# Kernel tuning notes

Measured on AMD Instinct MI355X. Metric: run time of the kernel, lower is better.

## Reference

```python
import jax, jax.numpy as jnp
import numpy as np

H = 3.0        # args.h smoothing length
N_NODES = 100000
DIM_HIDDEN = 128
D = 3


def setup_inputs() -> dict:
    key = jax.random.key(0)
    ks = jax.random.split(key, 10)
    E = 1600000
    v = jax.random.normal(ks[0], (N_NODES, D), dtype=jnp.float32)
    r_ij = jax.random.normal(ks[1], (E, D), dtype=jnp.float32)
    edge_index = jax.random.randint(ks[2], (2, E), 0, N_NODES, dtype=jnp.int64)
    # teacher MLP params: [1+D] -> dim_hidden -> dim_hidden -> 1
    def lin(k, fan_in, fan_out):
        bound = 1.0 / np.sqrt(fan_in)
        kw, kb = jax.random.split(k)
        W = jax.random.uniform(kw, (fan_out, fan_in), jnp.float32, -bound, bound)
        b = jax.random.uniform(kb, (fan_out,), jnp.float32, -bound, bound)
        return W, b
    W0, b0 = lin(ks[3], 1 + D, DIM_HIDDEN)
    W1, b1 = lin(ks[4], DIM_HIDDEN, DIM_HIDDEN)
    W2, b2 = lin(ks[5], DIM_HIDDEN, 1)
    return {"v": v, "r_ij": r_ij, "W0": W0, "b0": b0, "W1": W1, "b1": b1,
            "W2": W2, "b2": b2, "edge_index": edge_index}


def _teacher(x, W0, b0, W1, b1, W2, b2):
    x = jax.nn.silu(x @ W0.T + b0)
    x = jax.nn.silu(x @ W1.T + b1)
    return x @ W2.T + b2  # [E, 1]


def _scatter_mean(x, idx, n):
    s = jax.ops.segment_sum(x, idx, num_segments=n)
    c = jax.ops.segment_sum(jnp.ones((idx.shape[0], 1), x.dtype), idx, num_segments=n)
    return s / jnp.maximum(c, 1.0)


def reference(v, r_ij, W0, b0, W1, b1, W2, b2, edge_index):
    i = edge_index[0]
    j = edge_index[1]
    v_ij = v[i] - v[j]                                   # [E, D] gather-diff
    r_ = jnp.sqrt(jnp.sum(r_ij * r_ij, axis=-1, keepdims=True)) / H  # [E, 1]
    m_i = _teacher(jnp.concatenate([r_, v_ij], axis=-1), W0, b0, W1, b1, W2, b2)
    m_j = _teacher(jnp.concatenate([r_, -v_ij], axis=-1), W0, b0, W1, b1, W2, b2)
    S = _scatter_mean(m_i, i, N_NODES) + _scatter_mean(m_j, j, N_NODES)  # [N, 1]
    return S
```

## Files before the change

### kernel.cpp

```cpp
#include <hip/hip_runtime.h>

typedef unsigned short ushort_t;
typedef __bf16 bf16x8 __attribute__((ext_vector_type(8)));
typedef __bf16 bf16x2 __attribute__((ext_vector_type(2)));
typedef float f32x4 __attribute__((ext_vector_type(4)));

#define LOG2E 1.4426950408889634f
#define LN2   0.6931471805599453f

__device__ __forceinline__ ushort_t f2bf(float f) {
    unsigned u;
    __builtin_memcpy(&u, &f, 4);
    u += 0x7fffu + ((u >> 16) & 1u);
    return (ushort_t)(u >> 16);
}

__device__ __forceinline__ float silu2(float y) {
    float e = __builtin_amdgcn_exp2f(-y);
    return y * __builtin_amdgcn_rcpf(1.0f + e);
}

__device__ __forceinline__ float rdlane(float v, int l) {
    return __builtin_bit_cast(float, __builtin_amdgcn_readlane(__builtin_bit_cast(int, v), l));
}


#define CNT_UNIT 65536.0

__global__ __launch_bounds__(256, 3) void mlp_kernel(
    const float* __restrict__ v,
    const float* __restrict__ rij,
    const float* __restrict__ W0,
    const float* __restrict__ b0,
    const float* __restrict__ W1,
    const float* __restrict__ b1,
    const float* __restrict__ W2,
    const float* __restrict__ b2,
    const int* __restrict__ eidx,
    double* __restrict__ acc_i, double* __restrict__ acc_j,
    int E, int nchunks)
{
    __shared__ ushort_t sW1[16384];
    __shared__ ushort_t sH0[8192];

    const int tid  = threadIdx.x;
    const int lane = tid & 63;
    const int wave = tid >> 6;

    {
        int n = tid >> 1, half = tid & 1;
        const float* src = W1 + n * 128;
#pragma unroll
        for (int dk = 0; dk < 8; dk++) {
            int k0   = half * 64 + dk * 8;
            int frag = (n >> 4) * 4 + (k0 >> 5);
            int slot = (n & 15) + 16 * ((k0 >> 3) & 3);
            ushort_t tmp[8];
#pragma unroll
            for (int t = 0; t < 8; t++) tmp[t] = f2bf(src[k0 + t]);
            *(uint4*)(&sW1[frag * 512 + slot * 8]) = *(const uint4*)tmp;
        }
    }

    float4 w0q[2]; float b0v[2];
#pragma unroll
    for (int kk = 0; kk < 2; kk++) {
        int h = 2 * lane + kk;
        w0q[kk].x = W0[h * 4 + 0] * LOG2E;
        w0q[kk].y = W0[h * 4 + 1] * LOG2E;
        w0q[kk].z = W0[h * 4 + 2] * LOG2E;
        w0q[kk].w = W0[h * 4 + 3] * LOG2E;
        b0v[kk]   = b0[h] * LOG2E;
    }
    float b1v[8], w2v[8];
#pragma unroll
    for (int nt = 0; nt < 8; nt++) {
        int ccol = nt * 16 + (lane & 15);
        b1v[nt] = b1[ccol] * LOG2E;
        w2v[nt] = W2[ccol] * LN2;
    }
    const float b2f = b2[0];

    __syncthreads();

    const int q = lane >> 4, c = lane & 15, p = (lane >> 2) & 3, bsub = lane & 3;
    const int ple  = lane >> 2;
    const int comp = lane & 3;

    auto preload = [&](int ch, float& val_o, int& idx_o) {
        float val = 0.f; int idxr = 0;
        int pe = ch * 64 + wave * 16 + ple;
        if (ch < nchunks && pe < E) {
            if (comp == 3) {
                float r0 = rij[3 * pe], r1 = rij[3 * pe + 1], r2 = rij[3 * pe + 2];
                val = sqrtf(fmaf(r0, r0, fmaf(r1, r1, r2 * r2))) * (1.0f / 3.0f);
            } else {
                int i = eidx[pe], jj = eidx[E + pe];
                idxr = (comp == 1) ? jj : i;
                val = v[3 * i + comp] - v[3 * jj + comp];
            }
        }
        val_o = val; idx_o = idxr;
    };

    float val; int idxr;
    preload(blockIdx.x, val, idxr);

    for (int chunk = blockIdx.x; chunk < nchunks; chunk += gridDim.x) {
        const float val_cur = val;
        const int   idx_cur = idxr;
        preload(chunk + (int)gridDim.x, val, idxr);

        const int ebase = chunk * 64 + wave * 16;

        bf16x8 afr[2][4];
#pragma unroll
        for (int half = 0; half < 2; ++half) {
#pragma unroll
            for (int le = 0; le < 8; le++) {
                int se = half * 8 + le;
                float vx = rdlane(val_cur, se * 4 + 0);
                float vy = rdlane(val_cur, se * 4 + 1);
                float vz = rdlane(val_cur, se * 4 + 2);
                float rr = rdlane(val_cur, se * 4 + 3);
                float si_[2], sj_[2];
#pragma unroll
                for (int kk = 0; kk < 2; kk++) {
                    float cc = fmaf(w0q[kk].x, rr, b0v[kk]);
                    float dd = fmaf(w0q[kk].y, vx, fmaf(w0q[kk].z, vy, w0q[kk].w * vz));
                    si_[kk] = silu2(cc + dd);
                    sj_[kk] = silu2(cc - dd);
                }
                bf16x2 pki, pkj;
                pki[0] = (__bf16)si_[0]; pki[1] = (__bf16)si_[1];
                pkj[0] = (__bf16)sj_[0]; pkj[1] = (__bf16)sj_[1];
                int mi = 2 * le;
                int fr = wave * 4 + q;
                int sli = ((mi ^ q ^ (p << 2)) & 15) + (p << 4);
                int slj = (((mi + 1) ^ q ^ (p << 2)) & 15) + (p << 4);
                ((unsigned*)sH0)[fr * 256 + sli * 4 + bsub] = __builtin_bit_cast(unsigned, pki);
                ((unsigned*)sH0)[fr * 256 + slj * 4 + bsub] = __builtin_bit_cast(unsigned, pkj);
            }
#pragma unroll
            for (int ks = 0; ks < 4; ks++) {
                int sl_rd = (((lane & 15) ^ ks ^ (q << 2)) & 15) + 16 * q;
                afr[half][ks] = *(const bf16x8*)(&sH0[(wave * 4 + ks) * 512 + sl_rd * 8]);
            }
        }

        f32x4 acc[2][8];
#pragma unroll
        for (int t = 0; t < 2; t++)
#pragma unroll
            for (int nt = 0; nt < 8; nt++)
                acc[t][nt] = (f32x4){b1v[nt], b1v[nt], b1v[nt], b1v[nt]};

#pragma unroll
        for (int ks = 0; ks < 4; ks++) {
#pragma unroll
            for (int nt = 0; nt < 8; nt++) {
                bf16x8 bb = *(const bf16x8*)(&sW1[(nt * 4 + ks) * 512 + lane * 8]);
                acc[0][nt] = __builtin_amdgcn_mfma_f32_16x16x32_bf16(afr[0][ks], bb, acc[0][nt], 0, 0, 0);
                acc[1][nt] = __builtin_amdgcn_mfma_f32_16x16x32_bf16(afr[1][ks], bb, acc[1][nt], 0, 0, 0);
            }
        }

        float rs[2][4] = {{0.f, 0.f, 0.f, 0.f}, {0.f, 0.f, 0.f, 0.f}};
#pragma unroll
        for (int t = 0; t < 2; t++)
#pragma unroll
            for (int nt = 0; nt < 8; nt++)
#pragma unroll
                for (int r = 0; r < 4; r++) {
                    float x = acc[t][nt][r];
                    rs[t][r] = fmaf(silu2(x), w2v[nt], rs[t][r]);
                }
#pragma unroll
        for (int t = 0; t < 2; t++)
#pragma unroll
            for (int r = 0; r < 4; r++) {
                float s = rs[t][r];
                s += __shfl_xor(s, 1, 64);
                s += __shfl_xor(s, 2, 64);
                s += __shfl_xor(s, 4, 64);
                s += __shfl_xor(s, 8, 64);
                int el  = t * 8 + q * 2 + (r >> 1);
                int src = el * 4 + (r & 1);
                int node = __shfl(idx_cur, src, 64);
                int e = ebase + el;
                if (c == 0 && e < E) {
                    double contrib = (double)(s + b2f) + CNT_UNIT;
                    if (r & 1) atomicAdd(&acc_j[node], contrib);
                    else       atomicAdd(&acc_i[node], contrib);
                }
            }
    }
}

__global__ void finalize_kernel(const double* __restrict__ acc_i,
                                const double* __restrict__ acc_j,
                                float* __restrict__ out, int N)
{
    int n = blockIdx.x * 256 + threadIdx.x;
    if (n < N) {
        double ti = acc_i[n], tj = acc_j[n];
        double ci = rint(ti * (1.0 / CNT_UNIT));
        double cj = rint(tj * (1.0 / CNT_UNIT));
        double si = ti - ci * CNT_UNIT;
        double sj = tj - cj * CNT_UNIT;
        out[n] = (float)(si / fmax(ci, 1.0) + sj / fmax(cj, 1.0));
    }
}

extern "C" void kernel_launch(void* const* d_in, const int* in_sizes, int n_in,
                              void* d_out, int out_size, void* d_ws, size_t ws_size,
                              hipStream_t stream) {
    const float* v   = (const float*)d_in[0];
    const float* rij = (const float*)d_in[1];
    const float* W0  = (const float*)d_in[2];
    const float* b0  = (const float*)d_in[3];
    const float* W1  = (const float*)d_in[4];
    const float* b1  = (const float*)d_in[5];
    const float* W2  = (const float*)d_in[6];
    const float* b2  = (const float*)d_in[7];
    const int* eidx  = (const int*)d_in[8];

    const int E = in_sizes[1] / 3;
    const int N = out_size;

    double* acc_i = (double*)d_ws;
    double* acc_j = acc_i + N;

    hipMemsetAsync(d_ws, 0, (size_t)2 * N * sizeof(double), stream);

    int nchunks = (E + 63) / 64;
    int grid = nchunks < 768 ? nchunks : 768;
    mlp_kernel<<<grid, 256, 0, stream>>>(v, rij, W0, b0, W1, b1, W2, b2, eidx,
                                         acc_i, acc_j, E, nchunks);
    finalize_kernel<<<(N + 255) / 256, 256, 0, stream>>>(acc_i, acc_j,
                                                         (float*)d_out, N);
}
```

Before: 381.1 us.

## Batch SiLU reciprocals four-at-a-time and enlarge blocks to 512 threads

Replaces the per-element SiLU reciprocal with a shared reciprocal across four values (one rcp plus extra multiplies), clamping inputs so the product of denominators cannot overflow. Also doubles the block to 512 threads (8 waves, 128 edges per chunk), sharing the bf16 W1 tile in LDS across more waves and changing the grid to 512 blocks with launch bounds (512,4). The aim is to cut transcendental-unit pressure and amortize W1 staging, at the cost of extra VALU multiplies, a slight precision change, and a different occupancy and register budget.

```diff
diff --git a/kernel.cpp b/kernel.cpp
--- a/kernel.cpp
+++ b/kernel.cpp
@@ -15,9 +15,20 @@
     return (ushort_t)(u >> 16);
 }
 
-__device__ __forceinline__ float silu2(float y) {
-    float e = __builtin_amdgcn_exp2f(-y);
-    return y * __builtin_amdgcn_rcpf(1.0f + e);
+__device__ __forceinline__ void silu2x4(float y0, float y1, float y2, float y3,
+                                        float& o0, float& o1, float& o2, float& o3) {
+    float e0 = __builtin_amdgcn_exp2f(-fmaxf(y0, -30.0f));
+    float e1 = __builtin_amdgcn_exp2f(-fmaxf(y1, -30.0f));
+    float e2 = __builtin_amdgcn_exp2f(-fmaxf(y2, -30.0f));
+    float e3 = __builtin_amdgcn_exp2f(-fmaxf(y3, -30.0f));
+    float d0 = 1.0f + e0, d1 = 1.0f + e1, d2 = 1.0f + e2, d3 = 1.0f + e3;
+    float p01 = d0 * d1, p23 = d2 * d3;
+    float r   = __builtin_amdgcn_rcpf(p01 * p23);
+    float r01 = p23 * r, r23 = p01 * r;
+    o0 = y0 * (d1 * r01);
+    o1 = y1 * (d0 * r01);
+    o2 = y2 * (d3 * r23);
+    o3 = y3 * (d2 * r23);
 }
 
 __device__ __forceinline__ float rdlane(float v, int l) {
@@ -27,7 +38,7 @@
 
 #define CNT_UNIT 65536.0
 
-__global__ __launch_bounds__(256, 3) void mlp_kernel(
+__global__ __launch_bounds__(512, 4) void mlp_kernel(
     const float* __restrict__ v,
     const float* __restrict__ rij,
     const float* __restrict__ W0,
@@ -41,18 +52,18 @@
     int E, int nchunks)
 {
     __shared__ ushort_t sW1[16384];
-    __shared__ ushort_t sH0[8192];
+    __shared__ ushort_t sH0[16384];
 
     const int tid  = threadIdx.x;
     const int lane = tid & 63;
     const int wave = tid >> 6;
 
     {
-        int n = tid >> 1, half = tid & 1;
+        int n = tid >> 2, qr = tid & 3;
         const float* src = W1 + n * 128;
 #pragma unroll
-        for (int dk = 0; dk < 8; dk++) {
-            int k0   = half * 64 + dk * 8;
+        for (int dk = 0; dk < 4; dk++) {
+            int k0   = qr * 32 + dk * 8;
             int frag = (n >> 4) * 4 + (k0 >> 5);
             int slot = (n & 15) + 16 * ((k0 >> 3) & 3);
             ushort_t tmp[8];
@@ -89,7 +100,7 @@
 
     auto preload = [&](int ch, float& val_o, int& idx_o) {
         float val = 0.f; int idxr = 0;
-        int pe = ch * 64 + wave * 16 + ple;
+        int pe = ch * 128 + wave * 16 + ple;
         if (ch < nchunks && pe < E) {
             if (comp == 3) {
                 float r0 = rij[3 * pe], r1 = rij[3 * pe + 1], r2 = rij[3 * pe + 2];
@@ -111,7 +122,7 @@
         const int   idx_cur = idxr;
         preload(chunk + (int)gridDim.x, val, idxr);
 
-        const int ebase = chunk * 64 + wave * 16;
+        const int ebase = chunk * 128 + wave * 16;
 
         bf16x8 afr[2][4];
 #pragma unroll
@@ -123,17 +134,15 @@
                 float vy = rdlane(val_cur, se * 4 + 1);
                 float vz = rdlane(val_cur, se * 4 + 2);
                 float rr = rdlane(val_cur, se * 4 + 3);
-                float si_[2], sj_[2];
-#pragma unroll
-                for (int kk = 0; kk < 2; kk++) {
-                    float cc = fmaf(w0q[kk].x, rr, b0v[kk]);
-                    float dd = fmaf(w0q[kk].y, vx, fmaf(w0q[kk].z, vy, w0q[kk].w * vz));
-                    si_[kk] = silu2(cc + dd);
-                    sj_[kk] = silu2(cc - dd);
-                }
+                float cc0 = fmaf(w0q[0].x, rr, b0v[0]);
+                float dd0 = fmaf(w0q[0].y, vx, fmaf(w0q[0].z, vy, w0q[0].w * vz));
+                float cc1 = fmaf(w0q[1].x, rr, b0v[1]);
+                float dd1 = fmaf(w0q[1].y, vx, fmaf(w0q[1].z, vy, w0q[1].w * vz));
+                float s0, s1, s2, s3;
+                silu2x4(cc0 + dd0, cc0 - dd0, cc1 + dd1, cc1 - dd1, s0, s1, s2, s3);
                 bf16x2 pki, pkj;
-                pki[0] = (__bf16)si_[0]; pki[1] = (__bf16)si_[1];
-                pkj[0] = (__bf16)sj_[0]; pkj[1] = (__bf16)sj_[1];
+                pki[0] = (__bf16)s0; pki[1] = (__bf16)s2;
+                pkj[0] = (__bf16)s1; pkj[1] = (__bf16)s3;
                 int mi = 2 * le;
                 int fr = wave * 4 + q;
                 int sli = ((mi ^ q ^ (p << 2)) & 15) + (p << 4);
@@ -169,12 +178,15 @@
 #pragma unroll
         for (int t = 0; t < 2; t++)
 #pragma unroll
-            for (int nt = 0; nt < 8; nt++)
-#pragma unroll
-                for (int r = 0; r < 4; r++) {
-                    float x = acc[t][nt][r];
-                    rs[t][r] = fmaf(silu2(x), w2v[nt], rs[t][r]);
-                }
+            for (int nt = 0; nt < 8; nt++) {
+                float s0, s1, s2, s3;
+                silu2x4(acc[t][nt][0], acc[t][nt][1], acc[t][nt][2], acc[t][nt][3],
+                        s0, s1, s2, s3);
+                rs[t][0] = fmaf(s0, w2v[nt], rs[t][0]);
+                rs[t][1] = fmaf(s1, w2v[nt], rs[t][1]);
+                rs[t][2] = fmaf(s2, w2v[nt], rs[t][2]);
+                rs[t][3] = fmaf(s3, w2v[nt], rs[t][3]);
+            }
 #pragma unroll
         for (int t = 0; t < 2; t++)
 #pragma unroll
@@ -233,9 +245,9 @@
 
     hipMemsetAsync(d_ws, 0, (size_t)2 * N * sizeof(double), stream);
 
-    int nchunks = (E + 63) / 64;
-    int grid = nchunks < 768 ? nchunks : 768;
-    mlp_kernel<<<grid, 256, 0, stream>>>(v, rij, W0, b0, W1, b1, W2, b2, eidx,
+    int nchunks = (E + 127) / 128;
+    int grid = nchunks < 512 ? nchunks : 512;
+    mlp_kernel<<<grid, 512, 0, stream>>>(v, rij, W0, b0, W1, b1, W2, b2, eidx,
                                          acc_i, acc_j, E, nchunks);
     finalize_kernel<<<(N + 255) / 256, 256, 0, stream>>>(acc_i, acc_j,
                                                          (float*)d_out, N);
```

After: 492.1 us. 29.1% more time.

## Swap MFMA operands so hidden units map to rows, shrinking output reduction

Applied to the files above, without the earlier changes.

Swaps the A/B operands of the second-layer MFMA so each accumulator holds hidden units along rows and edge-rows along columns. The layer-2 dot product then reduces mostly within each lane's registers, needing only two cross-lane shuffles per output instead of four per register-slot, and cuts 16 shuffle/atomic iterations to 2. Bias and W2 move from per-lane register arrays to shared memory, read as float4 per tile, which frees registers at the cost of extra LDS reads inside the hot loop.

```diff
diff --git a/kernel.cpp b/kernel.cpp
--- a/kernel.cpp
+++ b/kernel.cpp
@@ -42,6 +42,8 @@
 {
     __shared__ ushort_t sW1[16384];
     __shared__ ushort_t sH0[8192];
+    __shared__ float    sB1[128];
+    __shared__ float    sW2[128];
 
     const int tid  = threadIdx.x;
     const int lane = tid & 63;
@@ -60,6 +62,10 @@
             for (int t = 0; t < 8; t++) tmp[t] = f2bf(src[k0 + t]);
             *(uint4*)(&sW1[frag * 512 + slot * 8]) = *(const uint4*)tmp;
         }
+    }
+    if (tid < 128) {
+        sB1[tid] = b1[tid] * LOG2E;
+        sW2[tid] = W2[tid] * LN2;
     }
 
     float4 w0q[2]; float b0v[2];
@@ -72,18 +78,12 @@
         w0q[kk].w = W0[h * 4 + 3] * LOG2E;
         b0v[kk]   = b0[h] * LOG2E;
     }
-    float b1v[8], w2v[8];
-#pragma unroll
-    for (int nt = 0; nt < 8; nt++) {
-        int ccol = nt * 16 + (lane & 15);
-        b1v[nt] = b1[ccol] * LOG2E;
-        w2v[nt] = W2[ccol] * LN2;
-    }
     const float b2f = b2[0];
 
     __syncthreads();
 
     const int q = lane >> 4, c = lane & 15, p = (lane >> 2) & 3, bsub = lane & 3;
+    const int q4 = q * 4;
     const int ple  = lane >> 2;
     const int comp = lane & 3;
 
@@ -123,17 +123,17 @@
                 float vy = rdlane(val_cur, se * 4 + 1);
                 float vz = rdlane(val_cur, se * 4 + 2);
                 float rr = rdlane(val_cur, se * 4 + 3);
-                float si_[2], sj_[2];
-#pragma unroll
-                for (int kk = 0; kk < 2; kk++) {
-                    float cc = fmaf(w0q[kk].x, rr, b0v[kk]);
-                    float dd = fmaf(w0q[kk].y, vx, fmaf(w0q[kk].z, vy, w0q[kk].w * vz));
-                    si_[kk] = silu2(cc + dd);
-                    sj_[kk] = silu2(cc - dd);
-                }
+                float cc0 = fmaf(w0q[0].x, rr, b0v[0]);
+                float dd0 = fmaf(w0q[0].y, vx, fmaf(w0q[0].z, vy, w0q[0].w * vz));
+                float cc1 = fmaf(w0q[1].x, rr, b0v[1]);
+                float dd1 = fmaf(w0q[1].y, vx, fmaf(w0q[1].z, vy, w0q[1].w * vz));
+                float s0 = silu2(cc0 + dd0);
+                float s1 = silu2(cc0 - dd0);
+                float s2 = silu2(cc1 + dd1);
+                float s3 = silu2(cc1 - dd1);
                 bf16x2 pki, pkj;
-                pki[0] = (__bf16)si_[0]; pki[1] = (__bf16)si_[1];
-                pkj[0] = (__bf16)sj_[0]; pkj[1] = (__bf16)sj_[1];
+                pki[0] = (__bf16)s0; pki[1] = (__bf16)s2;
+                pkj[0] = (__bf16)s1; pkj[1] = (__bf16)s3;
                 int mi = 2 * le;
                 int fr = wave * 4 + q;
                 int sli = ((mi ^ q ^ (p << 2)) & 15) + (p << 4);
@@ -148,52 +148,48 @@
             }
         }
 
-        f32x4 acc[2][8];
-#pragma unroll
-        for (int t = 0; t < 2; t++)
-#pragma unroll
-            for (int nt = 0; nt < 8; nt++)
-                acc[t][nt] = (f32x4){b1v[nt], b1v[nt], b1v[nt], b1v[nt]};
+        f32x4 acc[8][2];
+#pragma unroll
+        for (int mt = 0; mt < 8; mt++) {
+            f32x4 bq = *(const f32x4*)(&sB1[mt * 16 + q4]);
+            acc[mt][0] = bq;
+            acc[mt][1] = bq;
+        }
 
 #pragma unroll
         for (int ks = 0; ks < 4; ks++) {
 #pragma unroll
-            for (int nt = 0; nt < 8; nt++) {
-                bf16x8 bb = *(const bf16x8*)(&sW1[(nt * 4 + ks) * 512 + lane * 8]);
-                acc[0][nt] = __builtin_amdgcn_mfma_f32_16x16x32_bf16(afr[0][ks], bb, acc[0][nt], 0, 0, 0);
-                acc[1][nt] = __builtin_amdgcn_mfma_f32_16x16x32_bf16(afr[1][ks], bb, acc[1][nt], 0, 0, 0);
-            }
-        }
-
-        float rs[2][4] = {{0.f, 0.f, 0.f, 0.f}, {0.f, 0.f, 0.f, 0.f}};
-#pragma unroll
-        for (int t = 0; t < 2; t++)
-#pragma unroll
-            for (int nt = 0; nt < 8; nt++)
-#pragma unroll
-                for (int r = 0; r < 4; r++) {
-                    float x = acc[t][nt][r];
-                    rs[t][r] = fmaf(silu2(x), w2v[nt], rs[t][r]);
-                }
-#pragma unroll
-        for (int t = 0; t < 2; t++)
+            for (int mt = 0; mt < 8; mt++) {
+                bf16x8 bb = *(const bf16x8*)(&sW1[(mt * 4 + ks) * 512 + lane * 8]);
+                acc[mt][0] = __builtin_amdgcn_mfma_f32_16x16x32_bf16(bb, afr[0][ks], acc[mt][0], 0, 0, 0);
+                acc[mt][1] = __builtin_amdgcn_mfma_f32_16x16x32_bf16(bb, afr[1][ks], acc[mt][1], 0, 0, 0);
+            }
+        }
+
+        float rs0 = 0.f, rs1 = 0.f;
+#pragma unroll
+        for (int mt = 0; mt < 8; mt++) {
+            f32x4 wq = *(const f32x4*)(&sW2[mt * 16 + q4]);
 #pragma unroll
             for (int r = 0; r < 4; r++) {
-                float s = rs[t][r];
-                s += __shfl_xor(s, 1, 64);
-                s += __shfl_xor(s, 2, 64);
-                s += __shfl_xor(s, 4, 64);
-                s += __shfl_xor(s, 8, 64);
-                int el  = t * 8 + q * 2 + (r >> 1);
-                int src = el * 4 + (r & 1);
-                int node = __shfl(idx_cur, src, 64);
-                int e = ebase + el;
-                if (c == 0 && e < E) {
-                    double contrib = (double)(s + b2f) + CNT_UNIT;
-                    if (r & 1) atomicAdd(&acc_j[node], contrib);
-                    else       atomicAdd(&acc_i[node], contrib);
-                }
-            }
+                rs0 = fmaf(silu2(acc[mt][0][r]), wq[r], rs0);
+                rs1 = fmaf(silu2(acc[mt][1][r]), wq[r], rs1);
+            }
+        }
+#pragma unroll
+        for (int et = 0; et < 2; et++) {
+            float s = et ? rs1 : rs0;
+            s += __shfl_xor(s, 16, 64);
+            s += __shfl_xor(s, 32, 64);
+            int er   = et * 16 + c;
+            int node = __shfl(idx_cur, (er >> 1) * 4 + (er & 1), 64);
+            int e    = ebase + (er >> 1);
+            if (q == 0 && e < E) {
+                double contrib = (double)(s + b2f) + CNT_UNIT;
+                double* dst = (er & 1) ? acc_j : acc_i;
+                atomicAdd(&dst[node], contrib);
+            }
+        }
     }
 }
 
```

Result: slower. 1.258 ms (+230.1%).

## Move W1 bf16 fragments from LDS to global memory and raise occupancy

Applied to the files above, without the earlier changes.

A separate prep kernel converts W1 to bf16 in MFMA fragment order once and writes it to workspace. The main kernel then reads B fragments from global memory (L1/L2-cached) instead of LDS, which frees 32KB of shared memory per block. Launch bounds go from 3 to 4 blocks per CU and the grid from 768 to 1024 persistent blocks. The intent is more resident waves to hide latency, at the cost of 32 global loads per chunk per wave that replace LDS reads, plus one extra kernel launch.

```diff
diff --git a/kernel.cpp b/kernel.cpp
--- a/kernel.cpp
+++ b/kernel.cpp
@@ -27,12 +27,29 @@
 
 #define CNT_UNIT 65536.0
 
-__global__ __launch_bounds__(256, 3) void mlp_kernel(
+__global__ void prep_w1(const float* __restrict__ W1, ushort_t* __restrict__ gW1)
+{
+    int tid = threadIdx.x;
+    int n = tid >> 1, half = tid & 1;
+    const float* src = W1 + n * 128;
+#pragma unroll
+    for (int dk = 0; dk < 8; dk++) {
+        int k0   = half * 64 + dk * 8;
+        int frag = (n >> 4) * 4 + (k0 >> 5);
+        int slot = (n & 15) + 16 * ((k0 >> 3) & 3);
+        ushort_t tmp[8];
+#pragma unroll
+        for (int t = 0; t < 8; t++) tmp[t] = f2bf(src[k0 + t]);
+        *(uint4*)(&gW1[frag * 512 + slot * 8]) = *(const uint4*)tmp;
+    }
+}
+
+__global__ __launch_bounds__(256, 4) void mlp_kernel(
     const float* __restrict__ v,
     const float* __restrict__ rij,
     const float* __restrict__ W0,
     const float* __restrict__ b0,
-    const float* __restrict__ W1,
+    const ushort_t* __restrict__ gW1,
     const float* __restrict__ b1,
     const float* __restrict__ W2,
     const float* __restrict__ b2,
@@ -40,27 +57,11 @@
     double* __restrict__ acc_i, double* __restrict__ acc_j,
     int E, int nchunks)
 {
-    __shared__ ushort_t sW1[16384];
     __shared__ ushort_t sH0[8192];
 
     const int tid  = threadIdx.x;
     const int lane = tid & 63;
     const int wave = tid >> 6;
-
-    {
-        int n = tid >> 1, half = tid & 1;
-        const float* src = W1 + n * 128;
-#pragma unroll
-        for (int dk = 0; dk < 8; dk++) {
-            int k0   = half * 64 + dk * 8;
-            int frag = (n >> 4) * 4 + (k0 >> 5);
-            int slot = (n & 15) + 16 * ((k0 >> 3) & 3);
-            ushort_t tmp[8];
-#pragma unroll
-            for (int t = 0; t < 8; t++) tmp[t] = f2bf(src[k0 + t]);
-            *(uint4*)(&sW1[frag * 512 + slot * 8]) = *(const uint4*)tmp;
-        }
-    }
 
     float4 w0q[2]; float b0v[2];
 #pragma unroll
@@ -80,8 +81,7 @@
         w2v[nt] = W2[ccol] * LN2;
     }
     const float b2f = b2[0];
-
-    __syncthreads();
+    const ushort_t* gW1l = gW1 + lane * 8;
 
     const int q = lane >> 4, c = lane & 15, p = (lane >> 2) & 3, bsub = lane & 3;
     const int ple  = lane >> 2;
@@ -123,17 +123,17 @@
                 float vy = rdlane(val_cur, se * 4 + 1);
                 float vz = rdlane(val_cur, se * 4 + 2);
                 float rr = rdlane(val_cur, se * 4 + 3);
-                float si_[2], sj_[2];
-#pragma unroll
-                for (int kk = 0; kk < 2; kk++) {
-                    float cc = fmaf(w0q[kk].x, rr, b0v[kk]);
-                    float dd = fmaf(w0q[kk].y, vx, fmaf(w0q[kk].z, vy, w0q[kk].w * vz));
-                    si_[kk] = silu2(cc + dd);
-                    sj_[kk] = silu2(cc - dd);
-                }
+                float cc0 = fmaf(w0q[0].x, rr, b0v[0]);
+                float dd0 = fmaf(w0q[0].y, vx, fmaf(w0q[0].z, vy, w0q[0].w * vz));
+                float cc1 = fmaf(w0q[1].x, rr, b0v[1]);
+                float dd1 = fmaf(w0q[1].y, vx, fmaf(w0q[1].z, vy, w0q[1].w * vz));
+                float s0 = silu2(cc0 + dd0);
+                float s1 = silu2(cc0 - dd0);
+                float s2 = silu2(cc1 + dd1);
+                float s3 = silu2(cc1 - dd1);
                 bf16x2 pki, pkj;
-                pki[0] = (__bf16)si_[0]; pki[1] = (__bf16)si_[1];
-                pkj[0] = (__bf16)sj_[0]; pkj[1] = (__bf16)sj_[1];
+                pki[0] = (__bf16)s0; pki[1] = (__bf16)s2;
+                pkj[0] = (__bf16)s1; pkj[1] = (__bf16)s3;
                 int mi = 2 * le;
                 int fr = wave * 4 + q;
                 int sli = ((mi ^ q ^ (p << 2)) & 15) + (p << 4);
@@ -159,7 +159,7 @@
         for (int ks = 0; ks < 4; ks++) {
 #pragma unroll
             for (int nt = 0; nt < 8; nt++) {
-                bf16x8 bb = *(const bf16x8*)(&sW1[(nt * 4 + ks) * 512 + lane * 8]);
+                bf16x8 bb = *(const bf16x8*)(&gW1l[(nt * 4 + ks) * 512]);
                 acc[0][nt] = __builtin_amdgcn_mfma_f32_16x16x32_bf16(afr[0][ks], bb, acc[0][nt], 0, 0, 0);
                 acc[1][nt] = __builtin_amdgcn_mfma_f32_16x16x32_bf16(afr[1][ks], bb, acc[1][nt], 0, 0, 0);
             }
@@ -230,12 +230,15 @@
 
     double* acc_i = (double*)d_ws;
     double* acc_j = acc_i + N;
+    ushort_t* gW1 = (ushort_t*)(acc_j + N);
 
     hipMemsetAsync(d_ws, 0, (size_t)2 * N * sizeof(double), stream);
 
+    prep_w1<<<1, 256, 0, stream>>>(W1, gW1);
+
     int nchunks = (E + 63) / 64;
-    int grid = nchunks < 768 ? nchunks : 768;
-    mlp_kernel<<<grid, 256, 0, stream>>>(v, rij, W0, b0, W1, b1, W2, b2, eidx,
+    int grid = nchunks < 1024 ? nchunks : 1024;
+    mlp_kernel<<<grid, 256, 0, stream>>>(v, rij, W0, b0, gW1, b1, W2, b2, eidx,
                                          acc_i, acc_j, E, nchunks);
     finalize_kernel<<<(N + 255) / 256, 256, 0, stream>>>(acc_i, acc_j,
                                                          (float*)d_out, N);
```

New measurement: 1.316 ms. +245.4%, slower.
